# Performance work log

Hardware: AMD Instinct MI355X
Metric: run time of the kernel (lower is better)

Reference implementation:

```python
import jax, jax.numpy as jnp
import numpy as np

K = 3  # torch_geometric knn_interpolate default
EPS = 1e-16


def knn_interpolate(l_y, l_pos, h_pos):
    # squared distances [N_h, N_l]
    d2 = jnp.sum((h_pos[:, None, :] - l_pos[None, :, :]) ** 2, axis=-1)
    neg_d, idx = jax.lax.top_k(-d2, K)          # k nearest: idx [N_h, K]
    w = 1.0 / jnp.maximum(-neg_d, EPS)           # inverse squared-distance weights
    feats = l_y[idx]                             # [N_h, K, F] gather
    return jnp.sum(w[..., None] * feats, axis=1) / jnp.sum(w, axis=1, keepdims=True)


def mlp(x, W1, b1, W2, b2, W3, b3):
    x = jax.nn.relu(x @ W1 + b1)
    x = jax.nn.relu(x @ W2 + b2)
    return x @ W3 + b3


def setup_inputs() -> dict:
    key = jax.random.key(0)
    ks = jax.random.split(key, 8)
    N_h, N_l, H, O = 32768, 8192, 512, 128
    s1 = 1.0 / np.sqrt(H)
    return {
        "emb": jax.random.normal(ks[0], (N_h, H), jnp.float32),
        "l_y": jax.random.normal(ks[1], (N_l, O), jnp.float32),
        "l_pos": jax.random.uniform(ks[2], (N_l, 3), jnp.float32),
        "h_pos": jax.random.uniform(ks[3], (N_h, 3), jnp.float32),
        "W1": jax.random.normal(ks[4], (H, H), jnp.float32) * s1,
        "b1": jnp.zeros((H,), jnp.float32),
        "W2": jax.random.normal(ks[5], (H, H), jnp.float32) * s1,
        "b2": jnp.zeros((H,), jnp.float32),
        "W3": jax.random.normal(ks[6], (H, O), jnp.float32) * s1,
        "b3": jnp.zeros((O,), jnp.float32),
    }


def reference(emb, l_y, l_pos, h_pos, W1, b1, W2, b2, W3, b3):
    x = mlp(emb, W1, b1, W2, b2, W3, b3)
    return x + knn_interpolate(l_y, l_pos, h_pos)
```

## Files before the change

### kernel.cpp

```cpp
#include <hip/hip_runtime.h>
#include <stdint.h>

typedef __attribute__((ext_vector_type(4))) float f32x4;
typedef __attribute__((ext_vector_type(8))) short bf16x8;

#define AS1(p) ((const __attribute__((address_space(1))) void*)(p))
#define AS3(p) ((__attribute__((address_space(3))) void*)(p))

__device__ __forceinline__ unsigned short f2bf(float f){
  unsigned u = __builtin_bit_cast(unsigned, f);
  u += 0x7FFF + ((u >> 16) & 1);
  return (unsigned short)(u >> 16);
}

template<int N> __device__ __forceinline__ void waitcnt_vm(){
  if constexpr (N==0) asm volatile("s_waitcnt vmcnt(0)" ::: "memory");
  else if constexpr (N==2) asm volatile("s_waitcnt vmcnt(2)" ::: "memory");
  else if constexpr (N==3) asm volatile("s_waitcnt vmcnt(3)" ::: "memory");
  else if constexpr (N==4) asm volatile("s_waitcnt vmcnt(4)" ::: "memory");
  else if constexpr (N==6) asm volatile("s_waitcnt vmcnt(6)" ::: "memory");
}

#define GD 14
#define NL 8192

__device__ __forceinline__ int cellcoord(float x){
  int c = (int)(x * (float)GD);
  return min(GD-1, max(0, c));
}

__global__ __launch_bounds__(256) void k_pre(const float* __restrict__ W1,
                                             const float* __restrict__ W2,
                                             const float* __restrict__ W3,
                                             unsigned short* __restrict__ W1t,
                                             unsigned short* __restrict__ W2t,
                                             unsigned short* __restrict__ W3t,
                                             const float* __restrict__ l_pos,
                                             int* __restrict__ cellStart,
                                             float4* __restrict__ sorted){
  const int z = blockIdx.z;
  if (z == 3){
    if (blockIdx.x != 0 || blockIdx.y != 0) return;
    __shared__ int hist[4096];
    __shared__ int cur[4096];
    __shared__ int s[256];
    const int t = threadIdx.x;
    #pragma unroll
    for (int k = 0; k < 16; k++) hist[k*256 + t] = 0;
    __syncthreads();
    for (int k = 0; k < 32; k++){
      int i = k*256 + t;
      float x = l_pos[3*i], y = l_pos[3*i+1], zz = l_pos[3*i+2];
      int c = (cellcoord(zz)*GD + cellcoord(y))*GD + cellcoord(x);
      atomicAdd(&hist[c], 1);
    }
    __syncthreads();
    int loc[16]; int sum = 0;
    #pragma unroll
    for (int e = 0; e < 16; e++){ loc[e] = hist[t*16 + e]; sum += loc[e]; }
    s[t] = sum;
    __syncthreads();
    for (int off = 1; off < 256; off <<= 1){
      int val = (t >= off) ? s[t-off] : 0;
      __syncthreads();
      s[t] += val;
      __syncthreads();
    }
    int base = s[t] - sum;
    #pragma unroll
    for (int e = 0; e < 16; e++){
      cellStart[t*16 + e] = base;
      cur[t*16 + e] = base;
      base += loc[e];
    }
    __syncthreads();
    for (int k = 0; k < 32; k++){
      int i = k*256 + t;
      float x = l_pos[3*i], y = l_pos[3*i+1], zz = l_pos[3*i+2];
      int c = (cellcoord(zz)*GD + cellcoord(y))*GD + cellcoord(x);
      int slot = atomicAdd(&cur[c], 1);
      float4 q; q.x = x; q.y = y; q.z = zz; q.w = __int_as_float(i);
      sorted[slot] = q;
    }
    return;
  }
  const float* in; unsigned short* out; int R, C;
  if (z == 0){ in = W1; out = W1t; R = 512; C = 512; }
  else if (z == 1){ in = W2; out = W2t; R = 512; C = 512; }
  else { in = W3; out = W3t; R = 512; C = 128; if (blockIdx.x >= 4) return; }
  __shared__ float tile[32][33];
  int tx = threadIdx.x & 31, ty = threadIdx.x >> 5;
  int c0 = blockIdx.x*32, r0 = blockIdx.y*32;
  #pragma unroll
  for (int i = 0; i < 4; i++)
    tile[ty + i*8][tx] = in[(size_t)(r0 + ty + i*8)*C + c0 + tx];
  __syncthreads();
  #pragma unroll
  for (int i = 0; i < 4; i++)
    out[(size_t)(c0 + ty + i*8)*R + r0 + tx] = f2bf(tile[tx][ty + i*8]);
}

template<int BM, int NC, int TW, int MINW, bool AF32, bool RELU, bool OUTBF16, bool ADDOUT>
__global__ __launch_bounds__(TW, MINW) void k_gemm(const void* __restrict__ Av,
                                                   const unsigned short* __restrict__ Bt,
                                                   const float* __restrict__ bias,
                                                   void* __restrict__ out, int K){
  constexpr int WARPS_M = BM/64;
  constexpr int WARPS_N = (TW/64)/WARPS_M;
  constexpr int WN = NC/WARPS_N;
  constexpr int NI = WN/16;
  constexpr int IA = AF32 ? 0 : (BM*4)/TW;
  constexpr int IB = (NC*4)/TW;
  constexpr int LS = IA + IB;

  __shared__ short As[3][BM*32];
  __shared__ short Bs[3][NC*32];

  const int tid  = threadIdx.x;
  const int lane = tid & 63, wid = tid >> 6;
  const int wr = wid / WARPS_N, wc = wid % WARPS_N;
  const int l15 = lane & 15, lk = lane >> 4;
  const int bm = blockIdx.x, bn = blockIdx.y;

  const unsigned short* Bsrc[IB];
  #pragma unroll
  for (int q = 0; q < IB; q++){
    int row = q*(TW/4) + (tid >> 2);
    int ch  = (tid & 3) ^ ((row >> 1) & 3);
    Bsrc[q] = Bt + (size_t)bn*NC*K + (size_t)row*K + ch*8;
  }
  const unsigned short* Asrc16[IA > 0 ? IA : 1];
  if constexpr (!AF32){
    #pragma unroll
    for (int a = 0; a < IA; a++){
      int row = a*(TW/4) + (tid >> 2);
      int ch  = (tid & 3) ^ ((row >> 1) & 3);
      Asrc16[a] = (const unsigned short*)Av + (size_t)bm*BM*K + (size_t)row*K + ch*8;
    }
  }
  const float* A32 = (const float*)Av + (size_t)bm*BM*K + (size_t)(tid>>2)*K + (size_t)(tid&3)*8;
  const int woff = (tid >> 2)*32 + ((tid & 3) ^ (((tid >> 2) >> 1) & 3))*8;

#define STAGE_B(t_, bb_) do{ int k0_ = (t_) << 5; _Pragma("unroll") \
  for (int q = 0; q < IB; q++) \
    __builtin_amdgcn_global_load_lds(AS1(Bsrc[q] + k0_), AS3(&Bs[bb_][(q*(TW/4))*32 + tid*8]), 16, 0, 0); \
}while(0)
#define STAGE_A16(t_, bb_) do{ int k0_ = (t_) << 5; _Pragma("unroll") \
  for (int a = 0; a < IA; a++) \
    __builtin_amdgcn_global_load_lds(AS1(Asrc16[a] + k0_), AS3(&As[bb_][(a*(TW/4))*32 + tid*8]), 16, 0, 0); \
}while(0)
#define A_CONV_WRITE(bb_) do{ bf16x8 p_; _Pragma("unroll") \
  for (int j_ = 0; j_ < 4; j_++){ p_[j_] = (short)f2bf(ra0[j_]); p_[j_+4] = (short)f2bf(ra1[j_]); } \
  *(bf16x8*)&As[bb_][woff] = p_; \
}while(0)

  f32x4 acc[4][NI];
  #pragma unroll
  for (int i = 0; i < 4; i++)
    #pragma unroll
    for (int j = 0; j < NI; j++) acc[i][j] = (f32x4){0.f,0.f,0.f,0.f};

  const int nt = K >> 5;
  f32x4 ra0, ra1;

  if constexpr (AF32){
    ra0 = *(const f32x4*)(A32);
    ra1 = *(const f32x4*)(A32 + 4);
    STAGE_B(0, 0);
    STAGE_B(1, 1);
    waitcnt_vm<IB>();
    A_CONV_WRITE(0);
    asm volatile("s_waitcnt lgkmcnt(0)" ::: "memory");
  } else {
    STAGE_A16(0, 0); STAGE_B(0, 0);
    STAGE_A16(1, 1); STAGE_B(1, 1);
    waitcnt_vm<LS>();
  }
  __builtin_amdgcn_s_barrier();

  int b = 0;
  for (int t = 0; t < nt; ++t){
    bf16x8 af[4], bg[NI];
    #pragma unroll
    for (int i = 0; i < 4; i++){
      int R = wr*64 + i*16 + l15;
      af[i] = *(const bf16x8*)&As[b][R*32 + (lk ^ ((R >> 1) & 3))*8];
    }
    #pragma unroll
    for (int j = 0; j < NI; j++){
      int R = wc*WN + j*16 + l15;
      bg[j] = *(const bf16x8*)&Bs[b][R*32 + (lk ^ ((R >> 1) & 3))*8];
    }

    int b2 = b + 2; if (b2 >= 3) b2 -= 3;
    if constexpr (AF32){
      if (t + 1 < nt){
        int k1 = (t + 1) << 5;
        ra0 = *(const f32x4*)(A32 + k1);
        ra1 = *(const f32x4*)(A32 + k1 + 4);
      }
      if (t + 2 < nt) STAGE_B(t + 2, b2);
    } else {
      if (t + 2 < nt){ STAGE_A16(t + 2, b2); STAGE_B(t + 2, b2); }
    }

    __builtin_amdgcn_s_setprio(1);
    #pragma unroll
    for (int i = 0; i < 4; i++)
      #pragma unroll
      for (int j = 0; j < NI; j++)
        acc[i][j] = __builtin_amdgcn_mfma_f32_16x16x32_bf16(af[i], bg[j], acc[i][j], 0, 0, 0);
    __builtin_amdgcn_s_setprio(0);

    if (t + 2 < nt) waitcnt_vm<(AF32 ? IB : LS)>();
    else            waitcnt_vm<0>();
    if constexpr (AF32){
      if (t + 1 < nt){
        int wb = b + 1; if (wb >= 3) wb -= 3;
        A_CONV_WRITE(wb);
      }
    }
    asm volatile("s_waitcnt lgkmcnt(0)" ::: "memory");
    __builtin_amdgcn_s_barrier();
    b = (b + 1 == 3) ? 0 : b + 1;
  }
#undef STAGE_B
#undef STAGE_A16
#undef A_CONV_WRITE

  const int row0 = bm*BM + wr*64 + lk*4;
  const int col0 = bn*NC + wc*WN + l15;
  const int NOUT = NC*gridDim.y;
  #pragma unroll
  for (int i = 0; i < 4; i++){
    #pragma unroll
    for (int j = 0; j < NI; j++){
      int col = col0 + j*16;
      float bv = bias[col];
      #pragma unroll
      for (int r = 0; r < 4; r++){
        int row = row0 + i*16 + r;
        float v = acc[i][j][r] + bv;
        if (RELU) v = fmaxf(v, 0.f);
        if (ADDOUT) v = v + ((const float*)out)[(size_t)row*NOUT + col];
        if (OUTBF16) ((unsigned short*)out)[(size_t)row*NOUT + col] = f2bf(v);
        else         ((float*)out)[(size_t)row*NOUT + col] = v;
      }
    }
  }
}

#define KNN_INS(dv, gi) \
  if (gi != i0 && gi != i1 && gi != i2 && \
      (dv < d2 || (dv == d2 && gi < i2))){ \
    if (dv < d1 || (dv == d1 && gi < i1)){ \
      d2 = d1; i2 = i1; \
      if (dv < d0 || (dv == d0 && gi < i0)){ d1 = d0; i1 = i0; d0 = dv; i0 = gi; } \
      else { d1 = dv; i1 = gi; } \
    } else { d2 = dv; i2 = gi; } \
  }

#define KNN_MERGE16() \
  _Pragma("unroll") \
  for (int m = 1; m < 16; m <<= 1){ \
    float e0 = __shfl_xor(d0, m), e1 = __shfl_xor(d1, m), e2 = __shfl_xor(d2, m); \
    int   j0 = __shfl_xor(i0, m), j1 = __shfl_xor(i1, m), j2 = __shfl_xor(i2, m); \
    KNN_INS(e0, j0); KNN_INS(e1, j1); KNN_INS(e2, j2); \
  }

__global__ __launch_bounds__(256) void k_knn(const float* __restrict__ h_pos,
                                             const int* __restrict__ cellStart,
                                             const float4* __restrict__ sorted,
                                             const float* __restrict__ l_y,
                                             float* __restrict__ out){
  const int t = blockIdx.x*256 + threadIdx.x;
  const int h = t >> 4, sl = t & 15;
  const float hx = h_pos[3*h], hy = h_pos[3*h+1], hz = h_pos[3*h+2];
  const int cx = cellcoord(hx), cy = cellcoord(hy), cz = cellcoord(hz);
  const float cs = 1.0f/(float)GD;
  float d0 = 3e38f, d1 = 3e38f, d2 = 3e38f;
  int   i0 = 0x7fffffff, i1 = 0x7fffffff, i2 = 0x7fffffff;

  for (int ci = sl; ci < 27; ci += 16){
    int dz = ci/9 - 1, dy = (ci - (ci/9)*9)/3 - 1, dx = ci % 3 - 1;
    int zz = cz+dz, yy = cy+dy, xx = cx+dx;
    if ((unsigned)zz >= GD || (unsigned)yy >= GD || (unsigned)xx >= GD) continue;
    int c = (zz*GD + yy)*GD + xx;
    int p0 = cellStart[c], p1 = cellStart[c+1];
    for (int p = p0; p < p1; p++){
      float4 qq = sorted[p];
      float ddx = hx - qq.x, ddy = hy - qq.y, ddz = hz - qq.z;
      float d = fmaf(ddx, ddx, fmaf(ddy, ddy, ddz*ddz));
      int gi = __float_as_int(qq.w);
      KNN_INS(d, gi);
    }
  }
  KNN_MERGE16();

  for (int r = 2; r < GD; r++){
    int rp = r - 1;
    float B = 3e38f;
    if (cx - rp > 0)      B = fminf(B, hx - (float)(cx-rp)*cs);
    if (cx + rp + 1 < GD) B = fminf(B, (float)(cx+rp+1)*cs - hx);
    if (cy - rp > 0)      B = fminf(B, hy - (float)(cy-rp)*cs);
    if (cy + rp + 1 < GD) B = fminf(B, (float)(cy+rp+1)*cs - hy);
    if (cz - rp > 0)      B = fminf(B, hz - (float)(cz-rp)*cs);
    if (cz + rp + 1 < GD) B = fminf(B, (float)(cz+rp+1)*cs - hz);
    if (d2 <= B*B) break;

    int side = 2*r + 1, ss = side*side, tot = ss*side;
    for (int ci = sl; ci < tot; ci += 16){
      int dz = ci/ss - r;
      int rem = ci - (ci/ss)*ss;
      int dy = rem/side - r, dx = rem - (rem/side)*side - r;
      int adx = abs(dx), ady = abs(dy), adz = abs(dz);
      if (max(adx, max(ady, adz)) < r) continue;
      int zz = cz+dz, yy = cy+dy, xx = cx+dx;
      if ((unsigned)zz >= GD || (unsigned)yy >= GD || (unsigned)xx >= GD) continue;
      int c = (zz*GD + yy)*GD + xx;
      int p0 = cellStart[c], p1 = cellStart[c+1];
      for (int p = p0; p < p1; p++){
        float4 qq = sorted[p];
        float ddx = hx - qq.x, ddy = hy - qq.y, ddz = hz - qq.z;
        float d = fmaf(ddx, ddx, fmaf(ddy, ddy, ddz*ddz));
        int gi = __float_as_int(qq.w);
        KNN_INS(d, gi);
      }
    }
    KNN_MERGE16();
  }

  float w0 = 1.0f/fmaxf(d0, 1e-16f);
  float w1 = 1.0f/fmaxf(d1, 1e-16f);
  float w2 = 1.0f/fmaxf(d2, 1e-16f);
  float inv = 1.0f/(w0 + w1 + w2);
  const f32x4* ly4 = (const f32x4*)l_y;
  size_t b0 = (size_t)i0*32 + sl*2;
  size_t b1 = (size_t)i1*32 + sl*2;
  size_t b2 = (size_t)i2*32 + sl*2;
  f32x4 a0 = ly4[b0]*w0     + ly4[b1]*w1     + ly4[b2]*w2;
  f32x4 a1 = ly4[b0 + 1]*w0 + ly4[b1 + 1]*w1 + ly4[b2 + 1]*w2;
  size_t o = (size_t)h*32 + sl*2;
  ((f32x4*)out)[o]     = a0*inv;
  ((f32x4*)out)[o + 1] = a1*inv;
}

extern "C" void kernel_launch(void* const* d_in, const int* in_sizes, int n_in,
                              void* d_out, int out_size, void* d_ws, size_t ws_size,
                              hipStream_t stream){
  const float* emb   = (const float*)d_in[0];
  const float* l_y   = (const float*)d_in[1];
  const float* l_pos = (const float*)d_in[2];
  const float* h_pos = (const float*)d_in[3];
  const float* W1    = (const float*)d_in[4];
  const float* b1    = (const float*)d_in[5];
  const float* W2    = (const float*)d_in[6];
  const float* b2    = (const float*)d_in[7];
  const float* W3    = (const float*)d_in[8];
  const float* b3    = (const float*)d_in[9];

  const int M = 32768, H = 512;

  char* ws = (char*)d_ws;
  unsigned short* bufA = (unsigned short*)(ws);
  unsigned short* bufB = (unsigned short*)(ws + 33554432);
  unsigned short* W1t  = (unsigned short*)(ws + 67108864);
  unsigned short* W2t  = (unsigned short*)(ws + 67633152);
  unsigned short* W3t  = (unsigned short*)(ws + 68157440);
  int*    cellStart = (int*)   (ws + 68304896);
  float4* sorted    = (float4*)(ws + 68354048);

  k_pre<<<dim3(16, 16, 4), 256, 0, stream>>>(W1, W2, W3, W1t, W2t, W3t,
                                             l_pos, cellStart, sorted);

  k_knn<<<dim3(M*16/256), 256, 0, stream>>>(h_pos, cellStart, sorted, l_y, (float*)d_out);

  k_gemm<128, 256, 512, 4, true,  true,  true,  false><<<dim3(M/128, 2), 512, 0, stream>>>(emb,  W1t, b1, bufB, H);
  k_gemm<128, 256, 512, 4, false, true,  true,  false><<<dim3(M/128, 2), 512, 0, stream>>>(bufB, W2t, b2, bufA, H);
  k_gemm<64,  128, 256, 2, false, false, false, true ><<<dim3(M/64,  1), 256, 0, stream>>>(bufA, W3t, b3, d_out, H);
}
```

Measured before the change: 119.8 us.

## Fuse KNN interpolation into first GEMM launch via interleaved block roles

Merges the KNN kernel and the first MLP GEMM into one launch. Block IDs are interleaved so that one in three blocks runs a GEMM tile and the rest run KNN work with 512 threads each. The aim is to overlap the latency-bound KNN search with the compute-bound GEMM and to drop one kernel launch. In exchange, the KNN blocks now carry the GEMM's shared-memory footprint and launch bounds, which may reduce occupancy for KNN.

```diff
diff --git a/kernel.cpp b/kernel.cpp
--- a/kernel.cpp
+++ b/kernel.cpp
@@ -100,11 +100,12 @@
     out[(size_t)(c0 + ty + i*8)*R + r0 + tx] = f2bf(tile[tx][ty + i*8]);
 }
 
-template<int BM, int NC, int TW, int MINW, bool AF32, bool RELU, bool OUTBF16, bool ADDOUT>
-__global__ __launch_bounds__(TW, MINW) void k_gemm(const void* __restrict__ Av,
-                                                   const unsigned short* __restrict__ Bt,
-                                                   const float* __restrict__ bias,
-                                                   void* __restrict__ out, int K){
+template<int BM, int NC, int TW, bool AF32, bool RELU, bool OUTBF16, bool ADDOUT>
+__device__ __forceinline__ void gemm_core(int bm, int bn, int NOUT,
+                                          const void* __restrict__ Av,
+                                          const unsigned short* __restrict__ Bt,
+                                          const float* __restrict__ bias,
+                                          void* __restrict__ out, int K){
   constexpr int WARPS_M = BM/64;
   constexpr int WARPS_N = (TW/64)/WARPS_M;
   constexpr int WN = NC/WARPS_N;
@@ -120,7 +121,6 @@
   const int lane = tid & 63, wid = tid >> 6;
   const int wr = wid / WARPS_N, wc = wid % WARPS_N;
   const int l15 = lane & 15, lk = lane >> 4;
-  const int bm = blockIdx.x, bn = blockIdx.y;
 
   const unsigned short* Bsrc[IB];
   #pragma unroll
@@ -230,7 +230,6 @@
 
   const int row0 = bm*BM + wr*64 + lk*4;
   const int col0 = bn*NC + wc*WN + l15;
-  const int NOUT = NC*gridDim.y;
   #pragma unroll
   for (int i = 0; i < 4; i++){
     #pragma unroll
@@ -250,6 +249,15 @@
   }
 }
 
+template<int BM, int NC, int TW, int MINW, bool AF32, bool RELU, bool OUTBF16, bool ADDOUT>
+__global__ __launch_bounds__(TW, MINW) void k_gemm(const void* __restrict__ Av,
+                                                   const unsigned short* __restrict__ Bt,
+                                                   const float* __restrict__ bias,
+                                                   void* __restrict__ out, int K, int NOUT){
+  gemm_core<BM, NC, TW, AF32, RELU, OUTBF16, ADDOUT>(blockIdx.x, blockIdx.y, NOUT,
+                                                     Av, Bt, bias, out, K);
+}
+
 #define KNN_INS(dv, gi) \
   if (gi != i0 && gi != i1 && gi != i2 && \
       (dv < d2 || (dv == d2 && gi < i2))){ \
@@ -268,13 +276,12 @@
     KNN_INS(e0, j0); KNN_INS(e1, j1); KNN_INS(e2, j2); \
   }
 
-__global__ __launch_bounds__(256) void k_knn(const float* __restrict__ h_pos,
-                                             const int* __restrict__ cellStart,
-                                             const float4* __restrict__ sorted,
-                                             const float* __restrict__ l_y,
-                                             float* __restrict__ out){
-  const int t = blockIdx.x*256 + threadIdx.x;
-  const int h = t >> 4, sl = t & 15;
+__device__ __forceinline__ void knn_core(int h, int sl,
+                                         const float* __restrict__ h_pos,
+                                         const int* __restrict__ cellStart,
+                                         const float4* __restrict__ sorted,
+                                         const float* __restrict__ l_y,
+                                         float* __restrict__ out){
   const float hx = h_pos[3*h], hy = h_pos[3*h+1], hz = h_pos[3*h+2];
   const int cx = cellcoord(hx), cy = cellcoord(hy), cz = cellcoord(hz);
   const float cs = 1.0f/(float)GD;
@@ -345,6 +352,28 @@
   ((f32x4*)out)[o + 1] = a1*inv;
 }
 
+__global__ __launch_bounds__(512, 4) void k_g1knn(const float* __restrict__ emb,
+                                                  const unsigned short* __restrict__ W1t,
+                                                  const float* __restrict__ b1,
+                                                  unsigned short* __restrict__ bufB,
+                                                  const float* __restrict__ h_pos,
+                                                  const int* __restrict__ cellStart,
+                                                  const float4* __restrict__ sorted,
+                                                  const float* __restrict__ l_y,
+                                                  float* __restrict__ dout){
+  const int gid = blockIdx.x;
+  const int m3 = gid % 3;
+  if (m3 == 0){
+    int g = gid / 3;
+    gemm_core<128, 256, 512, true, true, true, false>(g >> 1, g & 1, 512,
+                                                      emb, W1t, b1, bufB, 512);
+  } else {
+    int k = (gid / 3)*2 + m3 - 1;
+    int t = threadIdx.x;
+    knn_core(k*32 + (t >> 4), t & 15, h_pos, cellStart, sorted, l_y, dout);
+  }
+}
+
 extern "C" void kernel_launch(void* const* d_in, const int* in_sizes, int n_in,
                               void* d_out, int out_size, void* d_ws, size_t ws_size,
                               hipStream_t stream){
@@ -373,9 +402,10 @@
   k_pre<<<dim3(16, 16, 4), 256, 0, stream>>>(W1, W2, W3, W1t, W2t, W3t,
                                              l_pos, cellStart, sorted);
 
-  k_knn<<<dim3(M*16/256), 256, 0, stream>>>(h_pos, cellStart, sorted, l_y, (float*)d_out);
-
-  k_gemm<128, 256, 512, 4, true,  true,  true,  false><<<dim3(M/128, 2), 512, 0, stream>>>(emb,  W1t, b1, bufB, H);
-  k_gemm<128, 256, 512, 4, false, true,  true,  false><<<dim3(M/128, 2), 512, 0, stream>>>(bufB, W2t, b2, bufA, H);
-  k_gemm<64,  128, 256, 2, false, false, false, true ><<<dim3(M/64,  1), 256, 0, stream>>>(bufA, W3t, b3, d_out, H);
-}
+  k_g1knn<<<dim3(1536), 512, 0, stream>>>(emb, W1t, b1, bufB,
+                                          h_pos, cellStart, sorted, l_y,
+                                          (float*)d_out);
+
+  k_gemm<128, 256, 512, 4, false, true,  true,  false><<<dim3(M/128, 2), 512, 0, stream>>>(bufB, W2t, b2, bufA, H, 512);
+  k_gemm<64,  128, 256, 2, false, false, false, true ><<<dim3(M/64,  1), 256, 0, stream>>>(bufA, W3t, b3, d_out, H, 128);
+}
```

After: 119.5 us (median of 3 runs). No clear change (-0.3%).
